# Kernel tuning notes

Hardware: AMD Instinct MI355X
Metric: run time of the kernel (lower is better)

## Reference

```python
import jax, jax.numpy as jnp
import numpy as np

# dims
B, N, D = 2, 4096, 384
NUM_HEADS, KEY_DIM, VALUE_DIM = 8, 48, 48
TOP_K = 128
IDX_HEADS, IDX_DIM = 2, 32
SCALE = KEY_DIM ** (-0.5)


def setup_inputs() -> dict:
    key = jax.random.key(0)
    ks = jax.random.split(key, 9)
    def xavier(k, shape):
        fan_in, fan_out = shape[0], shape[1]
        lim = (6.0 / (fan_in + fan_out)) ** 0.5
        return jax.random.uniform(k, shape, jnp.float32, -lim, lim)
    return {
        "x": jax.random.normal(ks[0], (B, N, D), jnp.float32),
        # lightning indexer params
        "wq_idx": xavier(ks[1], (D, IDX_HEADS * IDX_DIM)),
        "wk_idx": xavier(ks[2], (D, IDX_DIM)),
        "ww_idx": xavier(ks[3], (D, IDX_HEADS)),
        # attention params (stored as (in, out) for x @ W)
        "wq": xavier(ks[4], (D, NUM_HEADS * KEY_DIM)),
        "wk": xavier(ks[5], (D, KEY_DIM)),
        "wv": xavier(ks[6], (D, VALUE_DIM)),
        "wo": xavier(ks[7], (NUM_HEADS * VALUE_DIM, D)),
    }


def _forward(x, wq_idx, wk_idx, ww_idx, wq, wk, wv, wo):
    b, n, d = x.shape
    # ---- Lightning indexer: I[q,s] = sum_h w[q,h] * relu(qi[q,h] . ki[s]) ----
    qi = (x @ wq_idx).reshape(b, n, IDX_HEADS, IDX_DIM)      # (B,N,Hi,dki)
    ki = x @ wk_idx                                           # (B,N,dki)
    w_idx = x @ ww_idx                                        # (B,N,Hi)
    raw = jax.nn.relu(jnp.einsum('bqhd,bsd->bqhs', qi, ki))   # (B,Nq,Hi,Nk)
    index_scores = jnp.einsum('bqhs,bqh->bqs', raw, w_idx)    # (B,Nq,Nk)

    # ---- MQA projections ----
    q = (x @ wq).reshape(b, n, NUM_HEADS, KEY_DIM).transpose(0, 2, 1, 3)  # (B,H,N,dk)
    k = x @ wk                                                # (B,N,dk) single KV head
    v = x @ wv                                                # (B,N,dv)

    # ---- top-k select + gather ----
    kk = min(TOP_K, n)
    _, top_idx = jax.lax.top_k(index_scores, kk)              # (B,Nq,k)
    bidx = jnp.arange(b)[:, None, None]
    sel_k = k[bidx, top_idx]                                  # (B,Nq,k,dk)
    sel_v = v[bidx, top_idx]                                  # (B,Nq,k,dv)

    # ---- sparse attention over selected keys ----
    attn = jnp.einsum('bhqd,bqkd->bhqk', q, sel_k) * SCALE    # (B,H,Nq,k)
    probs = jax.nn.softmax(attn, axis=-1)
    out = jnp.einsum('bhqk,bqkd->bhqd', probs, sel_v)         # (B,H,Nq,dv)
    out = out.transpose(0, 2, 1, 3).reshape(b, n, NUM_HEADS * VALUE_DIM)
    return out @ wo                                           # (B,N,D)


def reference(x, wq_idx, wk_idx, ww_idx, wq, wk, wv, wo):
    return _forward(x, wq_idx, wk_idx, ww_idx, wq, wk, wv, wo)
```

## Files before the change

### kernel.cpp

```cpp
#include <hip/hip_runtime.h>
#include <math.h>

#define NB 2
#define NSEQ 4096
#define DMODEL 384
#define NH 8
#define DKQ 48
#define DV 48
#define TOPK 128
#define NQ (NB*NSEQ)

#define QKV_COLS 480
#define C_Q 0
#define C_K 384
#define C_V 432
#define IDX_COLS 128
#define P_QI 0
#define P_KI 64
#define P_W  96
#define ATT_SCALE 0.14433756729740643f

typedef double v4d  __attribute__((ext_vector_type(4)));
typedef float  f32x4 __attribute__((ext_vector_type(4)));
typedef short  s16x8 __attribute__((ext_vector_type(8)));

__device__ inline void bsplit(float v, unsigned short& h, unsigned short& l) {
    unsigned hb = __float_as_uint(v);
    unsigned short hi = (unsigned short)((hb + 0x7FFFu + ((hb >> 16) & 1u)) >> 16);
    float hf = __uint_as_float(((unsigned)hi) << 16);
    float r = v - hf;
    unsigned rb = __float_as_uint(r);
    unsigned short lo = (unsigned short)((rb + 0x7FFFu + ((rb >> 16) & 1u)) >> 16);
    h = hi; l = lo;
}

__global__ void k_split(const float* __restrict__ x,
                        unsigned short* __restrict__ xhi, unsigned short* __restrict__ xlo) {
    int i = blockIdx.x * 256 + threadIdx.x;
    if (i < NQ * DMODEL) {
        unsigned short h, l;
        bsplit(x[i], h, l);
        xhi[i] = h; xlo[i] = l;
    }
}

__global__ void k_concat(const float* __restrict__ wq_idx, const float* __restrict__ wk_idx,
                         const float* __restrict__ ww_idx, const float* __restrict__ wq,
                         const float* __restrict__ wk, const float* __restrict__ wv,
                         const float* __restrict__ wo,
                         unsigned short* __restrict__ WqT_hi, unsigned short* __restrict__ WqT_lo,
                         unsigned short* __restrict__ WoT_hi, unsigned short* __restrict__ WoT_lo,
                         float* __restrict__ Wi_cat) {
    int i = blockIdx.x * 256 + threadIdx.x;
    const int NQK = QKV_COLS * DMODEL;
    const int NWO = DMODEL * DMODEL;
    if (i < NQK) {
        int n = i / DMODEL, k = i % DMODEL;
        float v;
        if (n < 384)      v = wq[(size_t)k*384 + n];
        else if (n < 432) v = wk[(size_t)k*48 + (n-384)];
        else              v = wv[(size_t)k*48 + (n-432)];
        unsigned short h, l; bsplit(v, h, l);
        WqT_hi[i] = h; WqT_lo[i] = l;
    } else if (i < NQK + NWO) {
        int j = i - NQK;
        int n = j / DMODEL, k = j % DMODEL;
        float v = wo[(size_t)k*384 + n];
        unsigned short h, l; bsplit(v, h, l);
        WoT_hi[j] = h; WoT_lo[j] = l;
    } else if (i < NQK + NWO + DMODEL*IDX_COLS) {
        int j = i - NQK - NWO;
        int d = j / IDX_COLS, c = j % IDX_COLS;
        float v;
        if (c < 64)       v = wq_idx[d*64 + c];
        else if (c < 96)  v = wk_idx[d*32 + (c-64)];
        else if (c < 98)  v = ww_idx[d*2 + (c-96)];
        else              v = 0.f;
        Wi_cat[j] = v;
    }
}

#define GLDK 40
__global__ __launch_bounds__(256) void k_gemm_mfma(
        const unsigned short* __restrict__ Ahi, const unsigned short* __restrict__ Alo,
        const unsigned short* __restrict__ Bhi, const unsigned short* __restrict__ Blo,
        float* __restrict__ C, int N, int ldc) {
    __shared__ unsigned short At[2][128][GLDK];
    __shared__ unsigned short Bt[2][64][GLDK];
    const int t = threadIdx.x;
    const int lane = t & 63, wid = t >> 6;
    const int row0 = blockIdx.y * 128, col0 = blockIdx.x * 64;
    const int ml = lane & 15, kq = lane >> 4;
    const int wm = (wid & 1) * 64, wn = (wid >> 1) * 32;

    unsigned short mv = (unsigned short)(__float_as_uint((float)(ml + 1)) >> 16);
    unsigned short one = 0x3F80;
    s16x8 pa, pb;
    #pragma unroll
    for (int j = 0; j < 8; j++) { pa[j] = (short)mv; pb[j] = (short)one; }
    f32x4 zf = (f32x4){0.f, 0.f, 0.f, 0.f};
    f32x4 rowp = __builtin_amdgcn_mfma_f32_16x16x32_bf16(pa, pb, zf, 0, 0, 0);
    f32x4 colp = __builtin_amdgcn_mfma_f32_16x16x32_bf16(pb, pa, zf, 0, 0, 0);
    int rowm[4], colm[4];
    #pragma unroll
    for (int r = 0; r < 4; r++) {
        rowm[r] = (((int)(rowp[r] * 0.03125f + 0.5f)) - 1) & 15;
        colm[r] = (((int)(colp[r] * 0.03125f + 0.5f)) - 1) & 15;
    }

    f32x4 acc[4][2];
    #pragma unroll
    for (int mt = 0; mt < 4; mt++)
        #pragma unroll
        for (int nt = 0; nt < 2; nt++) acc[mt][nt] = zf;

    for (int k0 = 0; k0 < DMODEL; k0 += 32) {
        #pragma unroll
        for (int i = 0; i < 4; i++) {
            int ch = t + 256*i;
            int arr = ch >> 9, rem = ch & 511;
            int r = rem >> 2, p = rem & 3;
            const unsigned short* src = arr ? Alo : Ahi;
            *(int4*)&At[arr][r][p*8] = *(const int4*)(src + (size_t)(row0 + r)*DMODEL + k0 + p*8);
        }
        #pragma unroll
        for (int i = 0; i < 2; i++) {
            int ch = t + 256*i;
            int arr = ch >> 8, rem = ch & 255;
            int r = rem >> 2, p = rem & 3;
            const unsigned short* src = arr ? Blo : Bhi;
            int gc = col0 + r;
            int4 v = {0, 0, 0, 0};
            if (gc < N) v = *(const int4*)(src + (size_t)gc*DMODEL + k0 + p*8);
            *(int4*)&Bt[arr][r][p*8] = v;
        }
        __syncthreads();
        s16x8 af[4][2], bfr[2][2];
        #pragma unroll
        for (int mt = 0; mt < 4; mt++)
            #pragma unroll
            for (int h = 0; h < 2; h++)
                af[mt][h] = *(const s16x8*)&At[h][wm + mt*16 + ml][kq*8];
        #pragma unroll
        for (int nt = 0; nt < 2; nt++)
            #pragma unroll
            for (int h = 0; h < 2; h++)
                bfr[nt][h] = *(const s16x8*)&Bt[h][wn + nt*16 + ml][kq*8];
        #pragma unroll
        for (int mt = 0; mt < 4; mt++)
            #pragma unroll
            for (int nt = 0; nt < 2; nt++) {
                acc[mt][nt] = __builtin_amdgcn_mfma_f32_16x16x32_bf16(af[mt][0], bfr[nt][0], acc[mt][nt], 0, 0, 0);
                acc[mt][nt] = __builtin_amdgcn_mfma_f32_16x16x32_bf16(af[mt][0], bfr[nt][1], acc[mt][nt], 0, 0, 0);
                acc[mt][nt] = __builtin_amdgcn_mfma_f32_16x16x32_bf16(af[mt][1], bfr[nt][0], acc[mt][nt], 0, 0, 0);
            }
        __syncthreads();
    }
    #pragma unroll
    for (int mt = 0; mt < 4; mt++)
        #pragma unroll
        for (int nt = 0; nt < 2; nt++)
            #pragma unroll
            for (int r = 0; r < 4; r++) {
                int rr = row0 + wm + mt*16 + rowm[r];
                int cc = col0 + wn + nt*16 + colm[r];
                if (cc < N) C[(size_t)rr*ldc + cc] = acc[mt][nt][r];
            }
}

__global__ __launch_bounds__(256) void k_proj64(const float* __restrict__ A,
                                                const float* __restrict__ W,
                                                double* __restrict__ P) {
    __shared__ float At[16][32];
    __shared__ float Bt[16][IDX_COLS];
    const int t  = threadIdx.x;
    const int tx = t & 15;
    const int ty = t >> 4;
    const int row0 = blockIdx.x * 32;
    double acc[2][8] = {};

    for (int k0 = 0; k0 < DMODEL; k0 += 16) {
        if (t < 128) {
            int m = t >> 2, kc = t & 3;
            float4 a = *(const float4*)(A + (size_t)(row0 + m)*DMODEL + k0 + kc*4);
            At[kc*4+0][m] = a.x; At[kc*4+1][m] = a.y;
            At[kc*4+2][m] = a.z; At[kc*4+3][m] = a.w;
        }
        for (int i = 0; i < 2; i++) {
            int lin = t + i*256;
            int kk = lin >> 5, c4 = lin & 31;
            float4 b = *(const float4*)(W + (size_t)(k0+kk)*IDX_COLS + c4*4);
            *(float4*)&Bt[kk][c4*4] = b;
        }
        __syncthreads();
        for (int kk = 0; kk < 16; kk++) {
            float a2[2], b8[8];
            a2[0] = At[kk][ty*2]; a2[1] = At[kk][ty*2+1];
            *(float4*)&b8[0] = *(const float4*)&Bt[kk][tx*8];
            *(float4*)&b8[4] = *(const float4*)&Bt[kk][tx*8+4];
            for (int i = 0; i < 2; i++)
                for (int j = 0; j < 8; j++)
                    acc[i][j] += (double)a2[i] * (double)b8[j];
        }
        __syncthreads();
    }
    for (int i = 0; i < 2; i++)
        for (int j = 0; j < 8; j++)
            P[(size_t)(row0 + ty*2 + i)*IDX_COLS + tx*8 + j] = acc[i][j];
}

__global__ __launch_bounds__(256) void k_score_mfma(const double* __restrict__ P,
                                                    unsigned int* __restrict__ K32,
                                                    int qstart) {
    __shared__ double A0[32][33];
    __shared__ double A1[32][33];
    __shared__ double Bk[32][129];
    __shared__ double wsh[2][32];
    const int t = threadIdx.x;
    const int lane = t & 63;
    const int wid = t >> 6;
    const int g0 = qstart + blockIdx.y * 32;
    const int b  = g0 / NSEQ;
    const int s0 = blockIdx.x * 128;

    for (int i = 0; i < 8; i++) {
        int lin = t + i*256;
        int q = lin >> 6, c = lin & 63;
        double v = P[(size_t)(g0 + q)*IDX_COLS + P_QI + c];
        if (c < 32) A0[c][q] = v; else A1[c-32][q] = v;
    }
    for (int i = 0; i < 16; i++) {
        int lin = t + i*256;
        int s = lin >> 5, c = lin & 31;
        Bk[c][s] = P[(size_t)(b*NSEQ + s0 + s)*IDX_COLS + P_KI + c];
    }
    if (t < 64) wsh[t & 1][t >> 1] = P[(size_t)(g0 + (t >> 1))*IDX_COLS + P_W + (t & 1)];

    const int qw = (wid & 1) * 16;
    const int sw = (wid >> 1) * 64;
    const int ml = lane & 15;
    const int kl = lane >> 4;

    v4d zero = (v4d){0.0, 0.0, 0.0, 0.0};
    v4d rowp = __builtin_amdgcn_mfma_f64_16x16x4f64((double)(ml+1), 1.0, zero, 0, 0, 0);
    v4d colp = __builtin_amdgcn_mfma_f64_16x16x4f64(1.0, (double)(ml+1), zero, 0, 0, 0);
    int rowm[4], colm[4];
    #pragma unroll
    for (int r = 0; r < 4; r++) {
        rowm[r] = (((int)(rowp[r] * 0.25 + 0.5)) - 1) & 15;
        colm[r] = (((int)(colp[r] * 0.25 + 0.5)) - 1) & 15;
    }

    __syncthreads();

    v4d acc0[4], acc1[4];
    #pragma unroll
    for (int st = 0; st < 4; st++) { acc0[st] = zero; acc1[st] = zero; }

    #pragma unroll
    for (int k4 = 0; k4 < 8; k4++) {
        int k = k4*4 + kl;
        double a0 = A0[k][qw + ml];
        double a1 = A1[k][qw + ml];
        #pragma unroll
        for (int st = 0; st < 4; st++) {
            double bb = Bk[k][sw + st*16 + ml];
            acc0[st] = __builtin_amdgcn_mfma_f64_16x16x4f64(a0, bb, acc0[st], 0, 0, 0);
            acc1[st] = __builtin_amdgcn_mfma_f64_16x16x4f64(a1, bb, acc1[st], 0, 0, 0);
        }
    }

    #pragma unroll
    for (int reg = 0; reg < 4; reg++) {
        int q = qw + rowm[reg];
        double w0 = wsh[0][q], w1 = wsh[1][q];
        #pragma unroll
        for (int st = 0; st < 4; st++) {
            double sc = w0 * fmax(acc0[st][reg], 0.0) + w1 * fmax(acc1[st][reg], 0.0);
            size_t oidx = (size_t)(blockIdx.y*32 + q)*NSEQ + s0 + sw + st*16 + colm[reg];
            float sf = (float)sc;
            unsigned int ub = __float_as_uint(sf);
            unsigned int u = (ub & 0x80000000u) ? ~ub : (ub | 0x80000000u);
            K32[oidx] = u;
        }
    }
}

__global__ __launch_bounds__(256) void k_topk(const unsigned int* __restrict__ K32,
                                              int* __restrict__ IDX, int qstart) {
    __shared__ unsigned int pool[1024];
    __shared__ unsigned int wred[4];
    __shared__ unsigned int s_b, s_need, s_flag, s_cnt, s_n;
    unsigned int* CK = pool;
    int* CI = (int*)(pool + 512);
    const int t = threadIdx.x, lane = t & 63;
    const int wid = t >> 6;
    const int q = blockIdx.x;
    const unsigned int* krow = K32 + (size_t)q * NSEQ;
    int* orow = IDX + (size_t)(qstart + q) * TOPK;

    unsigned int kr[16];
    #pragma unroll
    for (int jj = 0; jj < 4; jj++) {
        uint4 v = *(const uint4*)(krow + (t*4 + 1024*jj));
        kr[jj*4+0] = v.x; kr[jj*4+1] = v.y; kr[jj*4+2] = v.z; kr[jj*4+3] = v.w;
    }
    unsigned int mymax = kr[0];
    #pragma unroll
    for (int j = 1; j < 16; j++) mymax = kr[j] > mymax ? kr[j] : mymax;
    const unsigned int p16 = mymax >> 16;

    unsigned int Tw = 0;
    #pragma unroll
    for (int bit = 15; bit >= 0; --bit) {
        unsigned int trial = Tw | (1u << bit);
        if (__popcll(__ballot(p16 >= trial)) >= 32) Tw = trial;
    }
    if (lane == 0) wred[wid] = Tw;
    if (t == 0) { s_cnt = 0; s_n = 0; s_need = TOPK; s_flag = 0; }
    __syncthreads();
    unsigned int T16 = wred[0];
    T16 = wred[1] < T16 ? wred[1] : T16;
    T16 = wred[2] < T16 ? wred[2] : T16;
    T16 = wred[3] < T16 ? wred[3] : T16;

    #pragma unroll
    for (int j = 0; j < 16; j++) {
        if ((kr[j] >> 16) >= T16) {
            unsigned int pos = atomicAdd(&s_n, 1u);
            if (pos < 512u) { CK[pos] = kr[j]; CI[pos] = (j >> 2)*1024 + t*4 + (j & 3); }
        }
    }
    __syncthreads();
    const unsigned int n = s_n;

    if (n <= 512u) {
        if (wid == 0) {
            unsigned int ck[8]; int ci[8]; bool cv[8];
            #pragma unroll
            for (int e = 0; e < 8; e++) {
                int id = lane + e*64;
                cv[e] = (unsigned int)id < n;
                ck[e] = cv[e] ? CK[id] : 0u;
                ci[e] = cv[e] ? CI[id] : 0;
            }
            unsigned int T = 0;
            for (int bit = 31; bit >= 0; --bit) {
                unsigned int trial = T | (1u << bit);
                unsigned int c = 0;
                #pragma unroll
                for (int e = 0; e < 8; e++)
                    c += (unsigned int)__popcll(__ballot(cv[e] && ck[e] >= trial));
                if (c >= (unsigned int)TOPK) T = trial;
            }
            unsigned int G = 0, E = 0;
            #pragma unroll
            for (int e = 0; e < 8; e++) {
                G += (unsigned int)__popcll(__ballot(cv[e] && ck[e] > T));
                E += (unsigned int)__popcll(__ballot(cv[e] && ck[e] == T));
            }
            const unsigned int need = (unsigned int)TOPK - G;
            const unsigned long long ltm = (1ull << lane) - 1ull;

            unsigned int cbase = 0;
            #pragma unroll
            for (int e = 0; e < 8; e++) {
                bool em = cv[e] && ck[e] > T;
                unsigned long long m = __ballot(em);
                if (em) orow[cbase + __popcll(m & ltm)] = ci[e];
                cbase += (unsigned int)__popcll(m);
            }
            if (E == need) {
                #pragma unroll
                for (int e = 0; e < 8; e++) {
                    bool em = cv[e] && ck[e] == T;
                    unsigned long long m = __ballot(em);
                    if (em) orow[cbase + __popcll(m & ltm)] = ci[e];
                    cbase += (unsigned int)__popcll(m);
                }
            } else {
                unsigned int r = 0;
                for (int bit = 11; bit >= 0; --bit) {
                    unsigned int trial = r | (1u << bit);
                    unsigned int c = 0;
                    #pragma unroll
                    for (int e = 0; e < 8; e++)
                        c += (unsigned int)__popcll(__ballot(cv[e] && ck[e] == T &&
                                 (unsigned int)ci[e] <= trial));
                    if (c <= need) r = trial;
                }
                #pragma unroll
                for (int e = 0; e < 8; e++) {
                    bool em = cv[e] && ck[e] == T && (unsigned int)ci[e] <= r;
                    unsigned long long m = __ballot(em);
                    if (em) orow[cbase + __popcll(m & ltm)] = ci[e];
                    cbase += (unsigned int)__popcll(m);
                }
            }
        }
        return;
    }

    unsigned int amask = 0;
    #pragma unroll
    for (int j = 0; j < 16; j++)
        if ((kr[j] >> 16) >= T16) amask |= (1u << j);

    unsigned int (*hist)[256] = (unsigned int (*)[256])pool;
    auto clearhist = [&]() {
        #pragma unroll
        for (int w = 0; w < 4; w++) hist[w][t] = 0;
        __syncthreads();
    };
    auto decide = [&]() {
        if (wid == 0) {
            unsigned int c[4];
            #pragma unroll
            for (int k2 = 0; k2 < 4; k2++)
                c[k2] = hist[0][lane*4+k2] + hist[1][lane*4+k2]
                      + hist[2][lane*4+k2] + hist[3][lane*4+k2];
            unsigned int run = c[0] + c[1] + c[2] + c[3];
            #pragma unroll
            for (int d2 = 1; d2 < 64; d2 <<= 1) {
                unsigned int v = __shfl_down(run, d2, 64);
                if (lane + d2 < 64) run += v;
            }
            unsigned int need = s_need;
            unsigned int Sb[5];
            Sb[0] = run; Sb[1] = run - c[0]; Sb[2] = Sb[1] - c[1];
            Sb[3] = Sb[2] - c[2]; Sb[4] = Sb[3] - c[3];
            #pragma unroll
            for (int j = 0; j < 4; j++) {
                if (Sb[j] >= need && Sb[j+1] < need) {
                    s_b = (unsigned int)(lane*4 + j);
                    s_need = need - Sb[j+1];
                    s_flag = (need - Sb[j+1] == c[j]) ? 1u : 0u;
                }
            }
        }
        __syncthreads();
    };

    #pragma unroll 1
    for (int level = 0; level < 4; ++level) {
        const int sh = 24 - 8*level;
        clearhist();
        #pragma unroll
        for (int j = 0; j < 16; j++) {
            if ((amask >> j) & 1u)
                atomicAdd(&hist[wid][(kr[j] >> sh) & 255u], 1u);
        }
        __syncthreads();
        decide();
        const unsigned int bstar = s_b;

        if (s_flag) {
            #pragma unroll
            for (int j = 0; j < 16; j++) {
                if (((amask >> j) & 1u) && (((kr[j] >> sh) & 255u) >= bstar))
                    orow[atomicAdd(&s_cnt, 1u)] = (j >> 2)*1024 + t*4 + (j & 3);
            }
            return;
        }
        unsigned int nm = 0;
        #pragma unroll
        for (int j = 0; j < 16; j++) {
            if ((amask >> j) & 1u) {
                unsigned int d = (kr[j] >> sh) & 255u;
                if (d > bstar) orow[atomicAdd(&s_cnt, 1u)] = (j >> 2)*1024 + t*4 + (j & 3);
                else if (d == bstar) nm |= (1u << j);
            }
        }
        amask = nm;
    }

    const unsigned int needF = s_need;
    unsigned int base = 0;
    #pragma unroll 1
    for (int jj = 0; jj < 4; jj++) {
        unsigned int m4 = (amask >> (jj*4)) & 0xFu;
        unsigned int cnt = __popc(m4);
        unsigned int inc = cnt;
        #pragma unroll
        for (int d2 = 1; d2 < 64; d2 <<= 1) {
            unsigned int v = __shfl_up(inc, d2, 64);
            if (lane >= d2) inc += v;
        }
        if (lane == 63) wred[wid] = inc;
        __syncthreads();
        unsigned int woff = 0;
        for (int w2 = 0; w2 < wid; w2++) woff += wred[w2];
        unsigned int T = wred[0] + wred[1] + wred[2] + wred[3];
        unsigned int p = base + woff + inc - cnt;
        #pragma unroll
        for (int c = 0; c < 4; c++) {
            if ((m4 >> c) & 1u) {
                if (p < needF) orow[atomicAdd(&s_cnt, 1u)] = jj*1024 + t*4 + c;
                p++;
            }
        }
        base += T;
        __syncthreads();
    }
}

__global__ __launch_bounds__(512, 6) void k_attn(const float* __restrict__ Y,
                                                 const int* __restrict__ IDX,
                                                 unsigned short* __restrict__ ctx_hi,
                                                 unsigned short* __restrict__ ctx_lo) {
    __shared__ float smem[TOPK * 64];
    __shared__ float qsh[NH*DKQ];
    __shared__ float prs[NH*TOPK];
    __shared__ int   idxs[TOPK];
    const int g = blockIdx.x;
    const int b = g / NSEQ;
    const int t = threadIdx.x;
    const int lane = t & 63, wid = t >> 6;

    if (t < TOPK) idxs[t] = IDX[(size_t)g*TOPK + t];
    if (t < NH*DKQ) qsh[t] = Y[(size_t)g*QKV_COLS + C_Q + t];
    __syncthreads();

    float4 vreg[3];
    #pragma unroll
    for (int i = 0; i < 3; i++) {
        int e = t + 512*i;
        int j = e / 12, p = e % 12;
        const float* src = Y + (size_t)(b*NSEQ + idxs[j])*QKV_COLS;
        *(float4*)&smem[j*64 + ((p ^ (j & 7)) * 4)] = *(const float4*)(src + C_K + p*4);
        vreg[i] = *(const float4*)(src + C_V + p*4);
    }
    __syncthreads();

    float4 qf[12];
    #pragma unroll
    for (int c = 0; c < 12; c++) qf[c] = *(const float4*)&qsh[wid*DKQ + c*4];
    float lo0 = 0.f, lo1 = 0.f;
    const int sw = (lane & 7);
    #pragma unroll
    for (int c = 0; c < 12; c++) {
        float4 k0 = *(const float4*)&smem[lane*64 + (c ^ sw) * 4];
        float4 k1 = *(const float4*)&smem[(lane + 64)*64 + (c ^ ((lane + 64) & 7)) * 4];
        float4 qv = qf[c];
        lo0 += qv.x*k0.x + qv.y*k0.y + qv.z*k0.z + qv.w*k0.w;
        lo1 += qv.x*k1.x + qv.y*k1.y + qv.z*k1.z + qv.w*k1.w;
    }
    lo0 *= ATT_SCALE; lo1 *= ATT_SCALE;
    float m = fmaxf(lo0, lo1);
    #pragma unroll
    for (int d = 32; d >= 1; d >>= 1) m = fmaxf(m, __shfl_xor(m, d, 64));
    float e0 = __expf(lo0 - m), e1 = __expf(lo1 - m);
    float sum = e0 + e1;
    #pragma unroll
    for (int d = 32; d >= 1; d >>= 1) sum += __shfl_xor(sum, d, 64);
    float inv = 1.0f / sum;
    prs[wid*TOPK + lane]      = e0 * inv;
    prs[wid*TOPK + lane + 64] = e1 * inv;
    __syncthreads();

    #pragma unroll
    for (int i = 0; i < 3; i++) {
        int e = t + 512*i;
        int j = e / 12, p = e % 12;
        #pragma unroll
        for (int c = 0; c < 4; c++) {
            int dd = p*4 + c;
            smem[dd*TOPK + (((j >> 2) ^ (dd & 31)) << 2) + (j & 3)] = ((const float*)&vreg[i])[c];
        }
    }
    __syncthreads();

    if (lane < DV) {
        const int dd = lane;
        const int dsw = dd & 31;
        float acc = 0.f;
        #pragma unroll
        for (int jb = 0; jb < 32; jb++) {
            float4 pv = *(const float4*)&prs[wid*TOPK + jb*4];
            float4 vt = *(const float4*)&smem[dd*TOPK + ((jb ^ dsw) << 2)];
            acc += pv.x*vt.x + pv.y*vt.y + pv.z*vt.z + pv.w*vt.w;
        }
        unsigned short ch, cl;
        bsplit(acc, ch, cl);
        ctx_hi[(size_t)g*(NH*DV) + wid*DV + dd] = ch;
        ctx_lo[(size_t)g*(NH*DV) + wid*DV + dd] = cl;
    }
}

extern "C" void kernel_launch(void* const* d_in, const int* in_sizes, int n_in,
                              void* d_out, int out_size, void* d_ws, size_t ws_size,
                              hipStream_t stream) {
    const float* x      = (const float*)d_in[0];
    const float* wq_idx = (const float*)d_in[1];
    const float* wk_idx = (const float*)d_in[2];
    const float* ww_idx = (const float*)d_in[3];
    const float* wq     = (const float*)d_in[4];
    const float* wk     = (const float*)d_in[5];
    const float* wv     = (const float*)d_in[6];
    const float* wo     = (const float*)d_in[7];
    float* out = (float*)d_out;
    char*  ws  = (char*)d_ws;

    size_t off = 0;
    auto carve = [&](size_t bytes) { size_t o = off; off = (off + bytes + 255) & ~(size_t)255; return o; };
    size_t oWqh = carve((size_t)QKV_COLS*DMODEL*2);
    size_t oWql = carve((size_t)QKV_COLS*DMODEL*2);
    size_t oWoh = carve((size_t)DMODEL*DMODEL*2);
    size_t oWol = carve((size_t)DMODEL*DMODEL*2);
    size_t oWi  = carve((size_t)DMODEL*IDX_COLS*4);
    size_t oXh  = carve((size_t)NQ*DMODEL*2);
    size_t oXl  = carve((size_t)NQ*DMODEL*2);
    size_t oY   = carve((size_t)NQ*QKV_COLS*4);
    size_t oP   = carve((size_t)NQ*IDX_COLS*8);
    size_t oIdx = carve((size_t)NQ*TOPK*4);
    size_t oCh  = carve((size_t)NQ*NH*DV*2);
    size_t oCl  = carve((size_t)NQ*NH*DV*2);
    size_t oKL  = off;

    int QC = NQ;
    while (QC > 32 && oKL + (size_t)QC*NSEQ*4 > ws_size) QC >>= 1;

    unsigned short* WqT_hi = (unsigned short*)(ws + oWqh);
    unsigned short* WqT_lo = (unsigned short*)(ws + oWql);
    unsigned short* WoT_hi = (unsigned short*)(ws + oWoh);
    unsigned short* WoT_lo = (unsigned short*)(ws + oWol);
    float*  Wi_cat = (float*)(ws + oWi);
    unsigned short* xhi = (unsigned short*)(ws + oXh);
    unsigned short* xlo = (unsigned short*)(ws + oXl);
    float*  Y      = (float*)(ws + oY);
    double* P      = (double*)(ws + oP);
    int*    IDX    = (int*)(ws + oIdx);
    unsigned short* ctx_hi = (unsigned short*)(ws + oCh);
    unsigned short* ctx_lo = (unsigned short*)(ws + oCl);
    unsigned int* K32 = (unsigned int*)(ws + oKL);

    int ncat = QKV_COLS*DMODEL + DMODEL*DMODEL + DMODEL*IDX_COLS;
    k_split<<<(NQ*DMODEL + 255)/256, 256, 0, stream>>>(x, xhi, xlo);
    k_concat<<<(ncat + 255)/256, 256, 0, stream>>>(wq_idx, wk_idx, ww_idx, wq, wk, wv, wo,
                                                   WqT_hi, WqT_lo, WoT_hi, WoT_lo, Wi_cat);
    k_gemm_mfma<<<dim3((QKV_COLS + 63)/64, NQ/128), 256, 0, stream>>>(xhi, xlo, WqT_hi, WqT_lo, Y, QKV_COLS, QKV_COLS);
    k_proj64<<<NQ/32, 256, 0, stream>>>(x, Wi_cat, P);
    for (int qs = 0; qs < NQ; qs += QC) {
        k_score_mfma<<<dim3(NSEQ/128, QC/32), 256, 0, stream>>>(P, K32, qs);
        k_topk<<<QC, 256, 0, stream>>>(K32, IDX, qs);
    }
    k_attn<<<NQ, 512, 0, stream>>>(Y, IDX, ctx_hi, ctx_lo);
    k_gemm_mfma<<<dim3(DMODEL/64, NQ/128), 256, 0, stream>>>(ctx_hi, ctx_lo, WoT_hi, WoT_lo, out, DMODEL, DMODEL);
}
```

Before: 443.4 us.

## Compute indexer scores with FP32 scalar FMAs instead of FP64 MFMA

The indexer score kernel stops using FP64 matrix-core MFMA. It now converts the query and key projections to float in shared memory and computes each score with per-thread FP32 dot products. Each thread keeps one key row in registers and loops over 16 queries, writing coalesced outputs along the sequence dimension. This removes the FP64 MFMA throughput cost and the lane-mapping tricks. The lower precision can change which keys win near-tied top-k selections.

Result: slower. 452.9 us (+2.1%).

```diff
diff --git a/kernel.cpp b/kernel.cpp
--- a/kernel.cpp
+++ b/kernel.cpp
@@ -209,80 +209,57 @@
             P[(size_t)(row0 + ty*2 + i)*IDX_COLS + tx*8 + j] = acc[i][j];
 }
 
+#define KSP 33
 __global__ __launch_bounds__(256) void k_score_mfma(const double* __restrict__ P,
                                                     unsigned int* __restrict__ K32,
                                                     int qstart) {
-    __shared__ double A0[32][33];
-    __shared__ double A1[32][33];
-    __shared__ double Bk[32][129];
-    __shared__ double wsh[2][32];
+    __shared__ float Qs[32][68];
+    __shared__ float Ks[128 * KSP];
+    __shared__ float wsh[2][32];
     const int t = threadIdx.x;
-    const int lane = t & 63;
-    const int wid = t >> 6;
     const int g0 = qstart + blockIdx.y * 32;
     const int b  = g0 / NSEQ;
     const int s0 = blockIdx.x * 128;
 
+    #pragma unroll
     for (int i = 0; i < 8; i++) {
         int lin = t + i*256;
         int q = lin >> 6, c = lin & 63;
-        double v = P[(size_t)(g0 + q)*IDX_COLS + P_QI + c];
-        if (c < 32) A0[c][q] = v; else A1[c-32][q] = v;
-    }
+        Qs[q][c] = (float)P[(size_t)(g0 + q)*IDX_COLS + P_QI + c];
+    }
+    #pragma unroll
     for (int i = 0; i < 16; i++) {
         int lin = t + i*256;
         int s = lin >> 5, c = lin & 31;
-        Bk[c][s] = P[(size_t)(b*NSEQ + s0 + s)*IDX_COLS + P_KI + c];
-    }
-    if (t < 64) wsh[t & 1][t >> 1] = P[(size_t)(g0 + (t >> 1))*IDX_COLS + P_W + (t & 1)];
-
-    const int qw = (wid & 1) * 16;
-    const int sw = (wid >> 1) * 64;
-    const int ml = lane & 15;
-    const int kl = lane >> 4;
-
-    v4d zero = (v4d){0.0, 0.0, 0.0, 0.0};
-    v4d rowp = __builtin_amdgcn_mfma_f64_16x16x4f64((double)(ml+1), 1.0, zero, 0, 0, 0);
-    v4d colp = __builtin_amdgcn_mfma_f64_16x16x4f64(1.0, (double)(ml+1), zero, 0, 0, 0);
-    int rowm[4], colm[4];
-    #pragma unroll
-    for (int r = 0; r < 4; r++) {
-        rowm[r] = (((int)(rowp[r] * 0.25 + 0.5)) - 1) & 15;
-        colm[r] = (((int)(colp[r] * 0.25 + 0.5)) - 1) & 15;
-    }
-
+        Ks[s*KSP + c] = (float)P[(size_t)(b*NSEQ + s0 + s)*IDX_COLS + P_KI + c];
+    }
+    if (t < 64) wsh[t & 1][t >> 1] = (float)P[(size_t)(g0 + (t >> 1))*IDX_COLS + P_W + (t & 1)];
     __syncthreads();
 
-    v4d acc0[4], acc1[4];
-    #pragma unroll
-    for (int st = 0; st < 4; st++) { acc0[st] = zero; acc1[st] = zero; }
-
-    #pragma unroll
-    for (int k4 = 0; k4 < 8; k4++) {
-        int k = k4*4 + kl;
-        double a0 = A0[k][qw + ml];
-        double a1 = A1[k][qw + ml];
-        #pragma unroll
-        for (int st = 0; st < 4; st++) {
-            double bb = Bk[k][sw + st*16 + ml];
-            acc0[st] = __builtin_amdgcn_mfma_f64_16x16x4f64(a0, bb, acc0[st], 0, 0, 0);
-            acc1[st] = __builtin_amdgcn_mfma_f64_16x16x4f64(a1, bb, acc1[st], 0, 0, 0);
-        }
-    }
-
-    #pragma unroll
-    for (int reg = 0; reg < 4; reg++) {
-        int q = qw + rowm[reg];
-        double w0 = wsh[0][q], w1 = wsh[1][q];
-        #pragma unroll
-        for (int st = 0; st < 4; st++) {
-            double sc = w0 * fmax(acc0[st][reg], 0.0) + w1 * fmax(acc1[st][reg], 0.0);
-            size_t oidx = (size_t)(blockIdx.y*32 + q)*NSEQ + s0 + sw + st*16 + colm[reg];
-            float sf = (float)sc;
-            unsigned int ub = __float_as_uint(sf);
-            unsigned int u = (ub & 0x80000000u) ? ~ub : (ub | 0x80000000u);
-            K32[oidx] = u;
-        }
+    const int s  = t & 127;
+    const int qh = t >> 7;
+    float kreg[32];
+    #pragma unroll
+    for (int c = 0; c < 32; c++) kreg[c] = Ks[s*KSP + c];
+
+    #pragma unroll 1
+    for (int qi = 0; qi < 16; qi++) {
+        const int q = qh*16 + qi;
+        float a0 = 0.f, a1 = 0.f;
+        #pragma unroll
+        for (int c = 0; c < 8; c++) {
+            float4 qv = *(const float4*)&Qs[q][c*4];
+            a0 += qv.x*kreg[c*4] + qv.y*kreg[c*4+1] + qv.z*kreg[c*4+2] + qv.w*kreg[c*4+3];
+        }
+        #pragma unroll
+        for (int c = 0; c < 8; c++) {
+            float4 qv = *(const float4*)&Qs[q][32 + c*4];
+            a1 += qv.x*kreg[c*4] + qv.y*kreg[c*4+1] + qv.z*kreg[c*4+2] + qv.w*kreg[c*4+3];
+        }
+        float sc = wsh[0][q]*fmaxf(a0, 0.f) + wsh[1][q]*fmaxf(a1, 0.f);
+        unsigned int ub = __float_as_uint(sc);
+        unsigned int u = (ub & 0x80000000u) ? ~ub : (ub | 0x80000000u);
+        K32[(size_t)(blockIdx.y*32 + q)*NSEQ + s0 + s] = u;
     }
 }
 
```
